# Performance work log

Measured on AMD Instinct MI355X. Metric: run time of the kernel, lower is better.

## Reference

```python
import jax, jax.numpy as jnp
import numpy as np

S, B, I, H, O = 4096, 64, 14, 256, 1


def _lstm_layer(xs, W_ih, W_hh, b_ih, b_hh, h, c):
    # Precompute input contribution for all timesteps in one big GEMM.
    # xs: [S, B, D_in] -> pre: [S, B, 4H]  (PyTorch gate order: i, f, g, o)
    pre = jnp.einsum('sbd,gd->sbg', xs, W_ih) + b_ih + b_hh

    def step(carry, px):
        h, c = carry
        gates = px + h @ W_hh.T  # [B, 4H]
        i, f, g, o = jnp.split(gates, 4, axis=-1)
        i = jax.nn.sigmoid(i)
        f = jax.nn.sigmoid(f)
        g = jnp.tanh(g)
        o = jax.nn.sigmoid(o)
        c = f * c + i * g
        h = o * jnp.tanh(c)
        return (h, c), h

    (_, _), hs = jax.lax.scan(step, (h, c), pre)
    return hs  # [S, B, H]


def setup_inputs() -> dict:
    key = jax.random.key(0)
    ks = jax.random.split(key, 14)
    s = 1.0 / np.sqrt(H)  # PyTorch LSTM init scale
    u = lambda k, shape: jax.random.uniform(k, shape, jnp.float32, -s, s)
    return {
        'x': jax.random.normal(ks[0], (S, B, I), jnp.float32),
        'h0': jax.random.normal(ks[1], (2, B, H), jnp.float32),
        'c0': jax.random.normal(ks[2], (2, B, H), jnp.float32),
        'W_ih0': u(ks[3], (4 * H, I)),
        'W_hh0': u(ks[4], (4 * H, H)),
        'b_ih0': u(ks[5], (4 * H,)),
        'b_hh0': u(ks[6], (4 * H,)),
        'W_ih1': u(ks[7], (4 * H, H)),
        'W_hh1': u(ks[8], (4 * H, H)),
        'b_ih1': u(ks[9], (4 * H,)),
        'b_hh1': u(ks[10], (4 * H,)),
        'W_fc': u(ks[11], (O, H)),
        'b_fc': u(ks[12], (O,)),
    }


def reference(x, h0, c0, W_ih0, W_hh0, b_ih0, b_hh0,
              W_ih1, W_hh1, b_ih1, b_hh1, W_fc, b_fc):
    hs0 = _lstm_layer(x, W_ih0, W_hh0, b_ih0, b_hh0, h0[0], c0[0])
    # dropout=0.4 between layers applies only in train mode; eval reference -> identity
    hs1 = _lstm_layer(hs0, W_ih1, W_hh1, b_ih1, b_hh1, h0[1], c0[1])
    out = jax.nn.relu(hs1)
    return out @ W_fc.T + b_fc  # [S, B, O]
```

## Files before the change

kernel.cpp:

```cpp
#include <hip/hip_runtime.h>


#define S_LEN 4096
#define BATCH 64
#define IN_DIM 14
#define HID 256
#define GATES 1024
#define K0 288
#define LDA0 300
#define K1 512
#define LDA1 524
#define GST 260

#define NFY(L, g, j, wv) ((((((L)*4 + (g)) * 4 + (j)) * 8) + (wv)) * 16)

typedef _Float16 half8 __attribute__((ext_vector_type(8)));
typedef _Float16 half4 __attribute__((ext_vector_type(4)));
typedef float f32x4 __attribute__((ext_vector_type(4)));
typedef unsigned long long u64;
typedef unsigned int u32;

__device__ __forceinline__ float sigf(float z) { return 1.0f / (1.0f + __expf(-z)); }
__device__ __forceinline__ float tanhf2(float z) { return 2.0f / (1.0f + __expf(-2.0f * z)) - 1.0f; }

__device__ __forceinline__ u64 aload(const u64* p) {
    return __hip_atomic_load(p, __ATOMIC_RELAXED, __HIP_MEMORY_SCOPE_AGENT);
}
__device__ __forceinline__ void astore(u64* p, u64 v) {
    __hip_atomic_store(p, v, __ATOMIC_RELAXED, __HIP_MEMORY_SCOPE_AGENT);
}
__device__ __forceinline__ u32 aload32(const u32* p) {
    return __hip_atomic_load(p, __ATOMIC_RELAXED, __HIP_MEMORY_SCOPE_AGENT);
}
__device__ __forceinline__ void astore32(u32* p, u32 v) {
    __hip_atomic_store(p, v, __ATOMIC_RELAXED, __HIP_MEMORY_SCOPE_AGENT);
}
__device__ __forceinline__ u32 packh2(float a, float b) {
    union { _Float16 h[2]; u32 u; } q;
    q.h[0] = (_Float16)a; q.h[1] = (_Float16)b;
    return q.u;
}
__device__ __forceinline__ half8 ldA(const _Float16* p) {
    half4 lo = *(const half4*)p;
    half4 hi = *(const half4*)(p + 4);
    return __builtin_shufflevector(lo, hi, 0, 1, 2, 3, 4, 5, 6, 7);
}
__device__ __forceinline__ void stA(_Float16* p, const float* src) {
    half4 lo, hi;
#pragma unroll
    for (int q2 = 0; q2 < 4; ++q2) { lo[q2] = (_Float16)src[q2]; hi[q2] = (_Float16)src[q2 + 4]; }
    *(half4*)p = lo;
    *(half4*)(p + 4) = hi;
}

__global__ void prep_weights(const float* __restrict__ Wih0, const float* __restrict__ Whh0,
                             const float* __restrict__ bih0, const float* __restrict__ bhh0,
                             const float* __restrict__ Wih1, const float* __restrict__ Whh1,
                             const float* __restrict__ bih1, const float* __restrict__ bhh1,
                             _Float16* __restrict__ wcat0, _Float16* __restrict__ wcat1,
                             float* __restrict__ b0, float* __restrict__ b1) {
    int idx0 = blockIdx.x * blockDim.x + threadIdx.x;
    int stride = gridDim.x * blockDim.x;
    for (int i = idx0; i < GATES * K0; i += stride) {
        int n = i / K0, k = i % K0;
        float v = 0.f;
        if (k < HID) v = Whh0[n * HID + k];
        else if (k < HID + IN_DIM) v = Wih0[n * IN_DIM + (k - HID)];
        wcat0[i] = (_Float16)v;
    }
    for (int i = idx0; i < GATES * K1; i += stride) {
        int n = i / K1, k = i % K1;
        float v = (k < HID) ? Whh1[n * HID + k] : Wih1[n * HID + (k - HID)];
        wcat1[i] = (_Float16)v;
    }
    for (int i = idx0; i < GATES; i += stride) {
        b0[i] = bih0[i] + bhh0[i];
        b1[i] = bih1[i] + bhh1[i];
    }
}

__global__ __launch_bounds__(512) void lstm_scan(
    const float* __restrict__ x, const float* __restrict__ h0g, const float* __restrict__ c0g,
    const _Float16* __restrict__ wcat0, const _Float16* __restrict__ wcat1,
    const float* __restrict__ b0, const float* __restrict__ b1,
    const float* __restrict__ wfc, const float* __restrict__ bfc,
    u64* __restrict__ h0ring, u64* __restrict__ h1ring,
    u32* __restrict__ nfy, u32* __restrict__ prog, float* __restrict__ out, int R0) {
    const int bi = blockIdx.x;
    const int g = bi & 7;
    if (g >= 4) return;
    const int role = bi >> 3;
    const int L = role >> 2;
    const int j = role & 3;

    const int tid = threadIdx.x;
    const int w = tid >> 6;
    const int lane = tid & 63;
    const int quad = lane >> 4;
    const int col = lane & 15;
    const int c0b = g * 16;
    const int pm = tid & 15;
    const int iu = tid >> 4;
    const int pu = iu * 2;
    const int gm = tid >> 5;
    const int gu = tid & 31;

    __shared__ __align__(16) _Float16 Ash[16 * LDA1];
    __shared__ float Gsh[16 * GST];
    __shared__ float WfS[HID];
    __shared__ u32 OwnH[512];

    u64* h0w = h0ring + (size_t)g * R0 * 2048;
    u64* h1w = h1ring + (size_t)g * 4 * 2048;
    const int R0m = R0 - 1;

    int peer[3];
    { int c = 0; for (int p = 0; p < 4; ++p) if (p != j) peer[c++] = p; }

    if (L == 0) {
        half8 wr[2][K0 / 32];
        float bs[2];
#pragma unroll
        for (int tt = 0; tt < 2; ++tt) {
            int t = w + 8 * tt;
            int n = (t >> 2) * 256 + j * 64 + (t & 3) * 16 + col;
            bs[tt] = b0[n];
            const _Float16* wp = wcat0 + (size_t)n * K0 + quad * 8;
#pragma unroll
            for (int kk = 0; kk < K0 / 32; ++kk) wr[tt][kk] = *(const half8*)(wp + kk * 32);
        }
        float cs0 = c0g[(size_t)(c0b + pm) * HID + j * 64 + pu];
        float cs1 = c0g[(size_t)(c0b + pm) * HID + j * 64 + pu + 1];
        {
            int m = tid >> 5, cw = tid & 31;
            const float* hp = h0g + (size_t)(c0b + m) * HID + cw * 8;
            float tmp[8];
#pragma unroll
            for (int q2 = 0; q2 < 8; ++q2) tmp[q2] = hp[q2];
            stA(&Ash[m * LDA0 + cw * 8], tmp);
            if (cw >= IN_DIM) Ash[m * LDA0 + HID + cw] = (_Float16)0.f;
        }
        const int xm = tid / IN_DIM, xd = tid - xm * IN_DIM;
        if (tid < 16 * IN_DIM)
            Ash[xm * LDA0 + HID + xd] = (_Float16)x[(size_t)(c0b + xm) * IN_DIM + xd];
        __syncthreads();

        for (int s = 0; s < S_LEN; ++s) {
            float xpre = 0.f;
            if (tid < 16 * IN_DIM && s + 1 < S_LEN)
                xpre = x[((size_t)(s + 1) * BATCH + c0b + xm) * IN_DIM + xd];
            const u64* ap[3];
            u64 vv[3] = {0, 0, 0};
            if (s > 0) {
                const u64* base = h0w + (size_t)((s - 1) & R0m) * 2048;
#pragma unroll
                for (int i = 0; i < 3; ++i) { ap[i] = base + peer[i] * 512 + tid; vv[i] = aload(ap[i]); }
            }
            if (w == 0) {
                bool act = false; const u32* np = nullptr; int tgt = 0;
                if (lane < 24) {
                    act = (s > 0); np = nfy + NFY(0, g, peer[lane >> 3], lane & 7); tgt = s;
                } else if (lane < 28) {
                    act = ((s & 7) == 0) && (s + 2 > R0);
                    np = prog + g * 4 + (lane - 24); tgt = s + 2 - R0;
                }
                bool ok = !act;
                for (;;) {
                    if (!ok) ok = ((int)aload32(np) >= tgt);
                    if (__all(ok)) break;
                    __builtin_amdgcn_s_sleep(1);
                }
            }
            __syncthreads();
            if (s > 0) {
#pragma unroll
                for (int i = 0; i < 3; ++i) {
                    while ((u32)(vv[i] >> 32) != (u32)s) vv[i] = aload(ap[i]);
                    *(u32*)&Ash[gm * LDA0 + peer[i] * 64 + 2 * gu] = (u32)vv[i];
                }
            }
            __syncthreads();
            f32x4 acc0 = {bs[0], bs[0], bs[0], bs[0]};
            f32x4 acc1 = {bs[1], bs[1], bs[1], bs[1]};
#pragma unroll
            for (int kk = 0; kk < K0 / 32; ++kk) {
                half8 av = ldA(&Ash[col * LDA0 + kk * 32 + quad * 8]);
                acc0 = __builtin_amdgcn_mfma_f32_16x16x32_f16(av, wr[0][kk], acc0, 0, 0, 0);
                acc1 = __builtin_amdgcn_mfma_f32_16x16x32_f16(av, wr[1][kk], acc1, 0, 0, 0);
            }
#pragma unroll
            for (int r = 0; r < 4; ++r) {
                Gsh[(quad * 4 + r) * GST + w * 16 + col] = acc0[r];
                Gsh[(quad * 4 + r) * GST + (w + 8) * 16 + col] = acc1[r];
            }
            __syncthreads();
            {
                float iv = sigf(Gsh[pm * GST + pu]);
                float fv = sigf(Gsh[pm * GST + 64 + pu]);
                float gv = tanhf2(Gsh[pm * GST + 128 + pu]);
                float ov = sigf(Gsh[pm * GST + 192 + pu]);
                cs0 = fv * cs0 + iv * gv;
                float ha = ov * tanhf2(cs0);
                iv = sigf(Gsh[pm * GST + pu + 1]);
                fv = sigf(Gsh[pm * GST + 64 + pu + 1]);
                gv = tanhf2(Gsh[pm * GST + 128 + pu + 1]);
                ov = sigf(Gsh[pm * GST + 192 + pu + 1]);
                cs1 = fv * cs1 + iv * gv;
                float hb = ov * tanhf2(cs1);
                u32 hw = packh2(ha, hb);
                *(u32*)&Ash[pm * LDA0 + j * 64 + pu] = hw;
                astore(h0w + (size_t)(s & R0m) * 2048 + j * 512 + (pm * 32 + iu),
                       (u64)hw | ((u64)(u32)(s + 1) << 32));
            }
            asm volatile("s_waitcnt vmcnt(0)" ::: "memory");
            if (lane == 0) astore32(nfy + NFY(0, g, j, w), (u32)(s + 1));
            if (tid < 16 * IN_DIM && s + 1 < S_LEN)
                Ash[xm * LDA0 + HID + xd] = (_Float16)xpre;
            __syncthreads();
        }
    } else {
        half8 wr[2][K1 / 32];
        float bs[2];
#pragma unroll
        for (int tt = 0; tt < 2; ++tt) {
            int t = w + 8 * tt;
            int n = (t >> 2) * 256 + j * 64 + (t & 3) * 16 + col;
            bs[tt] = b1[n];
            const _Float16* wp = wcat1 + (size_t)n * K1 + quad * 8;
#pragma unroll
            for (int kk = 0; kk < K1 / 32; ++kk) wr[tt][kk] = *(const half8*)(wp + kk * 32);
        }
        for (int i = tid; i < HID; i += 512) WfS[i] = wfc[i];
        const float bfcv = bfc[0];
        float cs0 = c0g[(size_t)(BATCH + c0b + pm) * HID + j * 64 + pu];
        float cs1 = c0g[(size_t)(BATCH + c0b + pm) * HID + j * 64 + pu + 1];
        {
            int m = tid >> 5, cw = tid & 31;
            const float* hp = h0g + (size_t)(BATCH + c0b + m) * HID + cw * 8;
            float tmp[8];
#pragma unroll
            for (int q2 = 0; q2 < 8; ++q2) tmp[q2] = hp[q2];
            stA(&Ash[m * LDA1 + cw * 8], tmp);
        }
        u32* progself = prog + g * 4 + j;
        const u64* hp0[4];
        u64 hv0[4];
#pragma unroll
        for (int p = 0; p < 4; ++p) { hp0[p] = h0w + p * 512 + tid; hv0[p] = aload(hp0[p]); }
        __syncthreads();

        for (int s = 0; s <= S_LEN; ++s) {
            const u64* ap[3];
            u64 vv[3] = {0, 0, 0};
            if (s > 0) {
                const u64* b1p = h1w + (size_t)((s - 1) & 3) * 2048;
#pragma unroll
                for (int i = 0; i < 3; ++i) { ap[i] = b1p + peer[i] * 512 + tid; vv[i] = aload(ap[i]); }
            }
            if (w == 0) {
                bool act = false; const u32* np = nullptr; int tgt = 0;
                if (lane < 24) {
                    act = (s > 0); np = nfy + NFY(1, g, peer[lane >> 3], lane & 7); tgt = s;
                } else if (lane < 56) {
                    int l2 = lane - 24;
                    act = (s < S_LEN); np = nfy + NFY(0, g, l2 >> 3, l2 & 7); tgt = s + 1;
                }
                bool ok = !act;
                for (;;) {
                    if (!ok) ok = ((int)aload32(np) >= tgt);
                    if (__all(ok)) break;
                    __builtin_amdgcn_s_sleep(1);
                }
            } else if (w == 7 && s >= 2) {
                int m = 4 * j + quad;
                float fa = 0.f;
#pragma unroll
                for (int k16 = 0; k16 < 16; ++k16) {
                    float hv = (float)Ash[m * LDA1 + col + 16 * k16];
                    fa += fmaxf(hv, 0.f) * WfS[col + 16 * k16];
                }
#pragma unroll
                for (int off = 1; off < 16; off <<= 1) fa += __shfl_xor(fa, off, 16);
                if (col == 0) out[(size_t)(s - 2) * BATCH + c0b + m] = fa + bfcv;
            }
            __syncthreads();
            if (s > 0) {
#pragma unroll
                for (int i = 0; i < 3; ++i) {
                    while ((u32)(vv[i] >> 32) != (u32)s) vv[i] = aload(ap[i]);
                    *(u32*)&Ash[gm * LDA1 + peer[i] * 64 + 2 * gu] = (u32)vv[i];
                }
                *(u32*)&Ash[gm * LDA1 + j * 64 + 2 * gu] = OwnH[tid];
            }
            if (s < S_LEN) {
#pragma unroll
                for (int p = 0; p < 4; ++p) {
                    while ((u32)(hv0[p] >> 32) != (u32)(s + 1)) hv0[p] = aload(hp0[p]);
                    *(u32*)&Ash[gm * LDA1 + HID + p * 64 + 2 * gu] = (u32)hv0[p];
                }
            }
            __syncthreads();
            if (s == S_LEN) {
                if (w == 7) {
                    int m = 4 * j + quad;
                    float fa = 0.f;
#pragma unroll
                    for (int k16 = 0; k16 < 16; ++k16) {
                        float hv = (float)Ash[m * LDA1 + col + 16 * k16];
                        fa += fmaxf(hv, 0.f) * WfS[col + 16 * k16];
                    }
#pragma unroll
                    for (int off = 1; off < 16; off <<= 1) fa += __shfl_xor(fa, off, 16);
                    if (col == 0) out[(size_t)(S_LEN - 1) * BATCH + c0b + m] = fa + bfcv;
                }
                break;
            }
            f32x4 acc0 = {bs[0], bs[0], bs[0], bs[0]};
            f32x4 acc1 = {bs[1], bs[1], bs[1], bs[1]};
#pragma unroll
            for (int kk = 0; kk < K1 / 32; ++kk) {
                half8 av = ldA(&Ash[col * LDA1 + kk * 32 + quad * 8]);
                acc0 = __builtin_amdgcn_mfma_f32_16x16x32_f16(av, wr[0][kk], acc0, 0, 0, 0);
                acc1 = __builtin_amdgcn_mfma_f32_16x16x32_f16(av, wr[1][kk], acc1, 0, 0, 0);
            }
#pragma unroll
            for (int r = 0; r < 4; ++r) {
                Gsh[(quad * 4 + r) * GST + w * 16 + col] = acc0[r];
                Gsh[(quad * 4 + r) * GST + (w + 8) * 16 + col] = acc1[r];
            }
            __syncthreads();
            {
                float iv = sigf(Gsh[pm * GST + pu]);
                float fv = sigf(Gsh[pm * GST + 64 + pu]);
                float gv = tanhf2(Gsh[pm * GST + 128 + pu]);
                float ov = sigf(Gsh[pm * GST + 192 + pu]);
                cs0 = fv * cs0 + iv * gv;
                float ha = ov * tanhf2(cs0);
                iv = sigf(Gsh[pm * GST + pu + 1]);
                fv = sigf(Gsh[pm * GST + 64 + pu + 1]);
                gv = tanhf2(Gsh[pm * GST + 128 + pu + 1]);
                ov = sigf(Gsh[pm * GST + 192 + pu + 1]);
                cs1 = fv * cs1 + iv * gv;
                float hb = ov * tanhf2(cs1);
                u32 hw = packh2(ha, hb);
                OwnH[pm * 32 + iu] = hw;
                astore(h1w + (size_t)(s & 3) * 2048 + j * 512 + (pm * 32 + iu),
                       (u64)hw | ((u64)(u32)(s + 1) << 32));
            }
            asm volatile("s_waitcnt vmcnt(0)" ::: "memory");
            if (lane == 0) astore32(nfy + NFY(1, g, j, w), (u32)(s + 1));
            if (s + 1 < S_LEN) {
#pragma unroll
                for (int p = 0; p < 4; ++p) {
                    hp0[p] = h0w + (size_t)((s + 1) & R0m) * 2048 + p * 512 + tid;
                    hv0[p] = aload(hp0[p]);
                }
            }
            if ((s & 7) == 7 && tid == 0) astore32(progself, (u32)(s + 1));
            __syncthreads();
        }
    }
}

extern "C" void kernel_launch(void* const* d_in, const int* in_sizes, int n_in,
                              void* d_out, int out_size, void* d_ws, size_t ws_size,
                              hipStream_t stream) {
    const float* x    = (const float*)d_in[0];
    const float* h0   = (const float*)d_in[1];
    const float* c0   = (const float*)d_in[2];
    const float* Wih0 = (const float*)d_in[3];
    const float* Whh0 = (const float*)d_in[4];
    const float* bih0 = (const float*)d_in[5];
    const float* bhh0 = (const float*)d_in[6];
    const float* Wih1 = (const float*)d_in[7];
    const float* Whh1 = (const float*)d_in[8];
    const float* bih1 = (const float*)d_in[9];
    const float* bhh1 = (const float*)d_in[10];
    const float* Wfc  = (const float*)d_in[11];
    const float* bfc  = (const float*)d_in[12];
    float* out = (float*)d_out;

    char* ws = (char*)d_ws;
    constexpr size_t OFF_WCAT0 = 0;
    constexpr size_t SZ_WCAT0 = (size_t)GATES * K0 * 2;
    constexpr size_t OFF_WCAT1 = OFF_WCAT0 + SZ_WCAT0;
    constexpr size_t SZ_WCAT1 = (size_t)GATES * K1 * 2;
    constexpr size_t OFF_B0 = OFF_WCAT1 + SZ_WCAT1;
    constexpr size_t OFF_B1 = OFF_B0 + 4096;
    constexpr size_t OFF_PROG = OFF_B1 + 4096;
    constexpr size_t SZ_PROG = 16384;
    constexpr size_t OFF_NFY = OFF_PROG + SZ_PROG;
    constexpr size_t SZ_NFY = 16384;
    constexpr size_t OFF_H1R = OFF_NFY + SZ_NFY;
    constexpr size_t SZ_H1R = (size_t)4 * 4 * 2048 * 8;
    constexpr size_t OFF_H0R = OFF_H1R + SZ_H1R;

    _Float16* wcat0 = (_Float16*)(ws + OFF_WCAT0);
    _Float16* wcat1 = (_Float16*)(ws + OFF_WCAT1);
    float* b0 = (float*)(ws + OFF_B0);
    float* b1 = (float*)(ws + OFF_B1);
    u32* prog = (u32*)(ws + OFF_PROG);
    u32* nfy = (u32*)(ws + OFF_NFY);
    u64* h1ring = (u64*)(ws + OFF_H1R);

    int R0 = 128;
    while (OFF_H0R + (size_t)4 * R0 * 2048 * 8 > ws_size && R0 > 16) R0 >>= 1;
    u64* h0ring = (u64*)(ws + OFF_H0R);

    hipMemsetAsync(prog, 0, SZ_PROG + SZ_NFY, stream);
    prep_weights<<<256, 256, 0, stream>>>(Wih0, Whh0, bih0, bhh0, Wih1, Whh1, bih1, bhh1,
                                          wcat0, wcat1, b0, b1);
    lstm_scan<<<64, 512, 0, stream>>>(x, h0, c0, wcat0, wcat1, b0, b1, Wfc, bfc,
                                      h0ring, h1ring, nfy, (u32*)prog, out, R0);
}
```

Measured before the change: 11.69 ms.

## Consolidate per-wave notify flags into one per-block flag line and split layer-1 GEMM

Replaces the per-wave notification counters and separate progress array with a single 16-word flag line per batch group, written once per block after a barrier. Layer-0 and layer-1 blocks now poll only 4–8 flags in one cache line instead of up to 56 scattered ones. Layer 1 also splits its K-loop so the input-side half (layer-0 h) is multiplied while it waits on peer layer-1 h, and the FC output moves to step s-1. This cuts polling and flag traffic on the serial recurrence path, at the cost of a coarser per-block signal after a full barrier plus extra vmcnt waits.

```diff
diff --git a/kernel.cpp b/kernel.cpp
--- a/kernel.cpp
+++ b/kernel.cpp
@@ -11,8 +11,6 @@
 #define K1 512
 #define LDA1 524
 #define GST 260
-
-#define NFY(L, g, j, wv) ((((((L)*4 + (g)) * 4 + (j)) * 8) + (wv)) * 16)
 
 typedef _Float16 half8 __attribute__((ext_vector_type(8)));
 typedef _Float16 half4 __attribute__((ext_vector_type(4)));
@@ -85,7 +83,7 @@
     const float* __restrict__ b0, const float* __restrict__ b1,
     const float* __restrict__ wfc, const float* __restrict__ bfc,
     u64* __restrict__ h0ring, u64* __restrict__ h1ring,
-    u32* __restrict__ nfy, u32* __restrict__ prog, float* __restrict__ out, int R0) {
+    u32* __restrict__ nfy, float* __restrict__ out, int R0) {
     const int bi = blockIdx.x;
     const int g = bi & 7;
     if (g >= 4) return;
@@ -108,10 +106,10 @@
     __shared__ __align__(16) _Float16 Ash[16 * LDA1];
     __shared__ float Gsh[16 * GST];
     __shared__ float WfS[HID];
-    __shared__ u32 OwnH[512];
 
     u64* h0w = h0ring + (size_t)g * R0 * 2048;
     u64* h1w = h1ring + (size_t)g * 4 * 2048;
+    u32* line = nfy + g * 16;
     const int R0m = R0 - 1;
 
     int peer[3];
@@ -158,11 +156,10 @@
             }
             if (w == 0) {
                 bool act = false; const u32* np = nullptr; int tgt = 0;
-                if (lane < 24) {
-                    act = (s > 0); np = nfy + NFY(0, g, peer[lane >> 3], lane & 7); tgt = s;
-                } else if (lane < 28) {
-                    act = ((s & 7) == 0) && (s + 2 > R0);
-                    np = prog + g * 4 + (lane - 24); tgt = s + 2 - R0;
+                if (lane < 4) {
+                    act = (s > 0) && (lane != j); np = line + lane; tgt = s;
+                } else if (lane < 8) {
+                    act = ((s & 7) == 0) && (s + 8 > R0); np = line + lane; tgt = s + 8 - R0;
                 }
                 bool ok = !act;
                 for (;;) {
@@ -208,15 +205,15 @@
                 cs1 = fv * cs1 + iv * gv;
                 float hb = ov * tanhf2(cs1);
                 u32 hw = packh2(ha, hb);
-                *(u32*)&Ash[pm * LDA0 + j * 64 + pu] = hw;
                 astore(h0w + (size_t)(s & R0m) * 2048 + j * 512 + (pm * 32 + iu),
                        (u64)hw | ((u64)(u32)(s + 1) << 32));
+                *(u32*)&Ash[pm * LDA0 + j * 64 + pu] = hw;
             }
             asm volatile("s_waitcnt vmcnt(0)" ::: "memory");
-            if (lane == 0) astore32(nfy + NFY(0, g, j, w), (u32)(s + 1));
             if (tid < 16 * IN_DIM && s + 1 < S_LEN)
                 Ash[xm * LDA0 + HID + xd] = (_Float16)xpre;
             __syncthreads();
+            if (tid == 0) astore32(line + j, (u32)(s + 1));
         }
     } else {
         half8 wr[2][K1 / 32];
@@ -242,7 +239,6 @@
             for (int q2 = 0; q2 < 8; ++q2) tmp[q2] = hp[q2];
             stA(&Ash[m * LDA1 + cw * 8], tmp);
         }
-        u32* progself = prog + g * 4 + j;
         const u64* hp0[4];
         u64 hv0[4];
 #pragma unroll
@@ -259,11 +255,10 @@
             }
             if (w == 0) {
                 bool act = false; const u32* np = nullptr; int tgt = 0;
-                if (lane < 24) {
-                    act = (s > 0); np = nfy + NFY(1, g, peer[lane >> 3], lane & 7); tgt = s;
-                } else if (lane < 56) {
-                    int l2 = lane - 24;
-                    act = (s < S_LEN); np = nfy + NFY(0, g, l2 >> 3, l2 & 7); tgt = s + 1;
+                if (lane < 4) {
+                    act = (s < S_LEN); np = line + lane; tgt = s + 1;
+                } else if (lane < 8) {
+                    act = (s > 0) && (lane - 4 != j); np = line + lane; tgt = s;
                 }
                 bool ok = !act;
                 for (;;) {
@@ -271,7 +266,34 @@
                     if (__all(ok)) break;
                     __builtin_amdgcn_s_sleep(1);
                 }
-            } else if (w == 7 && s >= 2) {
+            }
+            if (s < S_LEN) {
+#pragma unroll
+                for (int p = 0; p < 4; ++p) {
+                    while ((u32)(hv0[p] >> 32) != (u32)(s + 1)) hv0[p] = aload(hp0[p]);
+                    *(u32*)&Ash[gm * LDA1 + HID + p * 64 + 2 * gu] = (u32)hv0[p];
+                }
+            }
+            __syncthreads();
+            f32x4 acc0 = {bs[0], bs[0], bs[0], bs[0]};
+            f32x4 acc1 = {bs[1], bs[1], bs[1], bs[1]};
+            if (s < S_LEN) {
+#pragma unroll
+                for (int kk = 8; kk < 16; ++kk) {
+                    half8 av = ldA(&Ash[col * LDA1 + kk * 32 + quad * 8]);
+                    acc0 = __builtin_amdgcn_mfma_f32_16x16x32_f16(av, wr[0][kk], acc0, 0, 0, 0);
+                    acc1 = __builtin_amdgcn_mfma_f32_16x16x32_f16(av, wr[1][kk], acc1, 0, 0, 0);
+                }
+            }
+            if (s > 0) {
+#pragma unroll
+                for (int i = 0; i < 3; ++i) {
+                    while ((u32)(vv[i] >> 32) != (u32)s) vv[i] = aload(ap[i]);
+                    *(u32*)&Ash[gm * LDA1 + peer[i] * 64 + 2 * gu] = (u32)vv[i];
+                }
+            }
+            __syncthreads();
+            if (s >= 1 && w == 7) {
                 int m = 4 * j + quad;
                 float fa = 0.f;
 #pragma unroll
@@ -281,44 +303,11 @@
                 }
 #pragma unroll
                 for (int off = 1; off < 16; off <<= 1) fa += __shfl_xor(fa, off, 16);
-                if (col == 0) out[(size_t)(s - 2) * BATCH + c0b + m] = fa + bfcv;
-            }
-            __syncthreads();
-            if (s > 0) {
-#pragma unroll
-                for (int i = 0; i < 3; ++i) {
-                    while ((u32)(vv[i] >> 32) != (u32)s) vv[i] = aload(ap[i]);
-                    *(u32*)&Ash[gm * LDA1 + peer[i] * 64 + 2 * gu] = (u32)vv[i];
-                }
-                *(u32*)&Ash[gm * LDA1 + j * 64 + 2 * gu] = OwnH[tid];
-            }
-            if (s < S_LEN) {
-#pragma unroll
-                for (int p = 0; p < 4; ++p) {
-                    while ((u32)(hv0[p] >> 32) != (u32)(s + 1)) hv0[p] = aload(hp0[p]);
-                    *(u32*)&Ash[gm * LDA1 + HID + p * 64 + 2 * gu] = (u32)hv0[p];
-                }
-            }
-            __syncthreads();
-            if (s == S_LEN) {
-                if (w == 7) {
-                    int m = 4 * j + quad;
-                    float fa = 0.f;
-#pragma unroll
-                    for (int k16 = 0; k16 < 16; ++k16) {
-                        float hv = (float)Ash[m * LDA1 + col + 16 * k16];
-                        fa += fmaxf(hv, 0.f) * WfS[col + 16 * k16];
-                    }
-#pragma unroll
-                    for (int off = 1; off < 16; off <<= 1) fa += __shfl_xor(fa, off, 16);
-                    if (col == 0) out[(size_t)(S_LEN - 1) * BATCH + c0b + m] = fa + bfcv;
-                }
-                break;
-            }
-            f32x4 acc0 = {bs[0], bs[0], bs[0], bs[0]};
-            f32x4 acc1 = {bs[1], bs[1], bs[1], bs[1]};
-#pragma unroll
-            for (int kk = 0; kk < K1 / 32; ++kk) {
+                if (col == 0) out[(size_t)(s - 1) * BATCH + c0b + m] = fa + bfcv;
+            }
+            if (s == S_LEN) break;
+#pragma unroll
+            for (int kk = 0; kk < 8; ++kk) {
                 half8 av = ldA(&Ash[col * LDA1 + kk * 32 + quad * 8]);
                 acc0 = __builtin_amdgcn_mfma_f32_16x16x32_f16(av, wr[0][kk], acc0, 0, 0, 0);
                 acc1 = __builtin_amdgcn_mfma_f32_16x16x32_f16(av, wr[1][kk], acc1, 0, 0, 0);
@@ -343,12 +332,10 @@
                 cs1 = fv * cs1 + iv * gv;
                 float hb = ov * tanhf2(cs1);
                 u32 hw = packh2(ha, hb);
-                OwnH[pm * 32 + iu] = hw;
                 astore(h1w + (size_t)(s & 3) * 2048 + j * 512 + (pm * 32 + iu),
                        (u64)hw | ((u64)(u32)(s + 1) << 32));
-            }
-            asm volatile("s_waitcnt vmcnt(0)" ::: "memory");
-            if (lane == 0) astore32(nfy + NFY(1, g, j, w), (u32)(s + 1));
+                *(u32*)&Ash[pm * LDA1 + j * 64 + pu] = hw;
+            }
             if (s + 1 < S_LEN) {
 #pragma unroll
                 for (int p = 0; p < 4; ++p) {
@@ -356,8 +343,9 @@
                     hv0[p] = aload(hp0[p]);
                 }
             }
-            if ((s & 7) == 7 && tid == 0) astore32(progself, (u32)(s + 1));
-            __syncthreads();
+            asm volatile("s_waitcnt vmcnt(0)" ::: "memory");
+            __syncthreads();
+            if (tid == 0) astore32(line + 4 + j, (u32)(s + 1));
         }
     }
 }
@@ -387,10 +375,8 @@
     constexpr size_t SZ_WCAT1 = (size_t)GATES * K1 * 2;
     constexpr size_t OFF_B0 = OFF_WCAT1 + SZ_WCAT1;
     constexpr size_t OFF_B1 = OFF_B0 + 4096;
-    constexpr size_t OFF_PROG = OFF_B1 + 4096;
-    constexpr size_t SZ_PROG = 16384;
-    constexpr size_t OFF_NFY = OFF_PROG + SZ_PROG;
-    constexpr size_t SZ_NFY = 16384;
+    constexpr size_t OFF_NFY = OFF_B1 + 4096;
+    constexpr size_t SZ_NFY = 4096;
     constexpr size_t OFF_H1R = OFF_NFY + SZ_NFY;
     constexpr size_t SZ_H1R = (size_t)4 * 4 * 2048 * 8;
     constexpr size_t OFF_H0R = OFF_H1R + SZ_H1R;
@@ -399,7 +385,6 @@
     _Float16* wcat1 = (_Float16*)(ws + OFF_WCAT1);
     float* b0 = (float*)(ws + OFF_B0);
     float* b1 = (float*)(ws + OFF_B1);
-    u32* prog = (u32*)(ws + OFF_PROG);
     u32* nfy = (u32*)(ws + OFF_NFY);
     u64* h1ring = (u64*)(ws + OFF_H1R);
 
@@ -407,9 +392,9 @@
     while (OFF_H0R + (size_t)4 * R0 * 2048 * 8 > ws_size && R0 > 16) R0 >>= 1;
     u64* h0ring = (u64*)(ws + OFF_H0R);
 
-    hipMemsetAsync(prog, 0, SZ_PROG + SZ_NFY, stream);
+    hipMemsetAsync(nfy, 0, SZ_NFY, stream);
     prep_weights<<<256, 256, 0, stream>>>(Wih0, Whh0, bih0, bhh0, Wih1, Whh1, bih1, bhh1,
                                           wcat0, wcat1, b0, b1);
     lstm_scan<<<64, 512, 0, stream>>>(x, h0, c0, wcat0, wcat1, b0, b1, Wfc, bfc,
-                                      h0ring, h1ring, nfy, (u32*)prog, out, R0);
-}
+                                      h0ring, h1ring, nfy, out, R0);
+}
```

Measured after the change: 13.32 ms. 14.0% more time.
